# Performance work log

Hardware: AMD Instinct MI355X
Metric: run time of the kernel (lower is better)

Reference implementation:

```python
import jax, jax.numpy as jnp
import numpy as np
from jax.scipy.special import i0

# --- NUFFT adjoint (Kaiser-Bessel gridding) configuration ---
N = 512            # image side (image_shape)
K = 2 * N
M = 200_000        # n_measurements (visibilities)
B = 8              # batch of measurement vectors
J = 6              # gridding kernel width (plan uses (6, 6))
BETA = 2.34 * J


def setup_inputs() -> dict:
    key = jax.random.key(0)
    k1, k2, k3 = jax.random.split(key, 3)
    # uv coordinates in [-pi, pi) radians per pixel (standard NUFFT convention)
    uv = jax.random.uniform(k1, (M, 2), jnp.float32, -np.pi, np.pi)
    y_real = jax.random.normal(k2, (B, M), jnp.float32)
    y_imag = jax.random.normal(k3, (B, M), jnp.float32)
    weights = jnp.ones((M,), jnp.float32)  # measurement_weights
    return {"y_real": y_real, "y_imag": y_imag, "uv": uv, "weights": weights}


def _grid_1d(coord):
    """Per-axis gridding indices and Kaiser-Bessel weights.

    coord: (M,) frequencies in [-pi, pi). Returns idx (M, J) int32 grid
    columns (wrapped mod K) and w (M, J) float32 kernel weights.
    """
    k = coord / (2.0 * np.pi) * K            # grid units, in [-K/2, K/2)
    km = jnp.floor(k - J / 2.0)              # leftmost neighbor base
    j = jnp.arange(1, J + 1, dtype=k.dtype)
    pts = km[:, None] + j                    # (M, J) grid points covered
    d = k[:, None] - pts                     # signed distance, |d| <= J/2
    arg = jnp.maximum(1.0 - (2.0 * d / J) ** 2, 0.0)
    w = i0(BETA * jnp.sqrt(arg)) / i0(jnp.float32(BETA))
    idx = jnp.mod(pts, K).astype(jnp.int32)
    return idx, w.astype(jnp.float32)


def _deapod(n):
    """Gridding-correction (inverse FT of the KB kernel) at image pixels."""
    x = (jnp.arange(n, dtype=jnp.float32) - n / 2.0) / K
    t = BETA ** 2 - (np.pi * J * x) ** 2
    st = jnp.sqrt(jnp.abs(t))
    num = jnp.where(t > 0, jnp.sinh(st), jnp.sin(st))
    return num / jnp.maximum(st, 1e-6)


def reference(y_real, y_imag, uv, weights):
    y = (y_real + 1j * y_imag).astype(jnp.complex64) * weights  # (B, M)

    ix, wx = _grid_1d(uv[:, 0])  # (M, J)
    iy, wy = _grid_1d(uv[:, 1])  # (M, J)

    # Separable 6x6 kernel: outer products per measurement
    flat_idx = (ix[:, :, None] * K + iy[:, None, :]).reshape(-1)        # (M*J*J,)
    w2 = (wx[:, :, None] * wy[:, None, :]).reshape(M, J * J)            # (M, 36)
    vals = (y[:, :, None] * w2[None]).reshape(B, -1)                    # (B, M*36)

    # Scatter-add onto the oversampled grid (duplicate indices accumulate)
    grid = jnp.zeros((B, K * K), jnp.complex64).at[:, flat_idx].add(vals)
    grid = grid.reshape(B, K, K)

    # Unnormalized inverse FFT (adjoint of the forward FFT), shift to center
    img = jnp.fft.fftshift(jnp.fft.ifft2(grid), axes=(-2, -1)) * (K * K)

    # Crop central N x N region and de-apodize
    s = (K - N) // 2
    img_c = jnp.real(img[:, s:s + N, s:s + N])
    apod = _deapod(N)
    return img_c / (apod[:, None] * apod[None, :])
```

## Files before the change

### kernel.cpp

```cpp
#include <hip/hip_runtime.h>
#include <hip/hip_fp16.h>
#include <math.h>

#define KGRID 1024
#define NIMG  512
#define JW    6
#define BETAF 14.04f
#define NB    8
#define NBIN  16384
#define CAP   96

__device__ __forceinline__ float i0f_dev(float x) {
    float ax = fabsf(x);
    if (ax < 3.75f) {
        float z = ax * (1.0f / 3.75f);
        z = z * z;
        return 1.0f + z * (3.5156229f + z * (3.0899424f + z * (1.2067492f +
               z * (0.2659732f + z * (0.0360768f + z * 0.0045813f)))));
    } else {
        float z = 3.75f / ax;
        float p = 0.39894228f + z * (0.01328592f + z * (0.00225319f + z * (-0.00157565f +
                  z * (0.00916281f + z * (-0.02057706f + z * (0.02635537f +
                  z * (-0.01647633f + z * 0.00392377f)))))));
        return expf(ax) * rsqrtf(ax) * p;
    }
}

__global__ __launch_bounds__(256) void prep_kernel(
    const float* __restrict__ yr, const float* __restrict__ yi,
    const float* __restrict__ uv, const float* __restrict__ wts,
    float4* __restrict__ yF4, float4* __restrict__ pnt,
    int* __restrict__ cnt, int* __restrict__ list, int M)
{
    int m = blockIdx.x * 256 + threadIdx.x;
    if (m >= M) return;

    if (m == 0) {
        float4 z = make_float4(0.f, 0.f, 0.f, 0.f);
        #pragma unroll
        for (int q = 0; q < 4; q++) { pnt[(size_t)M * 4 + q] = z; yF4[(size_t)M * 4 + q] = z; }
    }

    float u = uv[2 * m], v = uv[2 * m + 1];
    const float c2g = (float)KGRID / 6.283185307179586f;
    float kx = u * c2g, ky = v * c2g;
    float kmx = floorf(kx - 3.0f), kmy = floorf(ky - 3.0f);
    int x0m = (((int)kmx + 1) + 1024) & 1023;
    int y0m = (((int)kmy + 1) + 1024) & 1023;

    int txA = x0m >> 3, txB = (txA + 1) & 127;
    int tyA = y0m >> 3, tyB = (tyA + 1) & 127;
    bool bx = (x0m & 7) >= 3;
    bool by = (y0m & 7) >= 3;
    int b0 = (txA << 7) | tyA;
    int b1 = (txA << 7) | tyB;
    int b2 = (txB << 7) | tyA;
    int b3 = (txB << 7) | tyB;
    int s0 = atomicAdd(&cnt[b0], 1);
    int s1 = by ? atomicAdd(&cnt[b1], 1) : -1;
    int s2 = bx ? atomicAdd(&cnt[b2], 1) : -1;
    int s3 = (bx && by) ? atomicAdd(&cnt[b3], 1) : -1;

    float inv = 1.0f / i0f_dev(BETAF);
    float s2c = inv * inv;
    float sc = wts[m] * s2c;

    float wx[JW], wy[JW];
    #pragma unroll
    for (int j = 0; j < JW; j++) {
        float dx = kx - kmx - 1.0f - (float)j;
        float rx = dx * (1.0f / 3.0f);
        float ax = fmaxf(1.0f - rx * rx, 0.0f);
        wx[j] = i0f_dev(BETAF * sqrtf(ax)) * sc;
        float dy = ky - kmy - 1.0f - (float)j;
        float ry = dy * (1.0f / 3.0f);
        float ay = fmaxf(1.0f - ry * ry, 0.0f);
        wy[j] = i0f_dev(BETAF * sqrtf(ay));
    }

    float4* p = pnt + (size_t)m * 4;
    p[0] = make_float4(wx[0], wx[1], wx[2], wx[3]);
    p[1] = make_float4(wx[4], wx[5], __int_as_float(x0m), __int_as_float(y0m));
    p[2] = make_float4(wy[0], wy[1], wy[2], wy[3]);
    p[3] = make_float4(wy[4], wy[5], 0.0f, 0.0f);

    #pragma unroll
    for (int bp = 0; bp < 4; bp++) {
        int bb = 2 * bp;
        yF4[(size_t)m * 4 + bp] = make_float4(
            yr[(size_t)bb * M + m],       yi[(size_t)bb * M + m],
            yr[(size_t)(bb + 1) * M + m], yi[(size_t)(bb + 1) * M + m]);
    }

    if ((unsigned)s0 < CAP) list[b0 * CAP + s0] = m;
    if ((unsigned)s1 < CAP) list[b1 * CAP + s1] = m;
    if ((unsigned)s2 < CAP) list[b2 * CAP + s2] = m;
    if ((unsigned)s3 < CAP) list[b3 * CAP + s3] = m;
}

__global__ __launch_bounds__(256) void grid_tile(
    const float* __restrict__ pnt1, const float4* __restrict__ yF4,
    const int* __restrict__ cnt, const int* __restrict__ list,
    __half2* __restrict__ gH, int M)
{
    int lane = threadIdx.x & 63;
    int wid  = threadIdx.x >> 6;
    int tile = blockIdx.x * 4 + wid;
    int tx0 = (tile >> 7) << 3;
    int ty0 = (tile & 127) << 3;
    int lx = lane >> 3, ly = lane & 7;
    int slot = lane & 15;

    float2 acc[NB];
    #pragma unroll
    for (int b = 0; b < NB; b++) acc[b] = make_float2(0.f, 0.f);

    int n = cnt[tile]; if (n > CAP) n = CAP;
    const int* lst = list + tile * CAP;

    int lv0 = (lane < n) ? lst[lane] : M;
    int lv1 = (64 + lane < n && 64 + lane < CAP) ? lst[64 + lane] : M;

    #define FETCH_M(i) __builtin_amdgcn_readlane(((i) < 64) ? lv0 : lv1, (i) & 63)

    int   mA = FETCH_M(0), mB = FETCH_M(1), mC = FETCH_M(2);
    float pwA = pnt1[(size_t)mA * 16 + slot];
    float pwB = pnt1[(size_t)mB * 16 + slot];
    float pwC = pnt1[(size_t)mC * 16 + slot];
    float4 yA0 = yF4[(size_t)mA * 4 + 0], yA1 = yF4[(size_t)mA * 4 + 1],
           yA2 = yF4[(size_t)mA * 4 + 2], yA3 = yF4[(size_t)mA * 4 + 3];
    float4 yB0 = yF4[(size_t)mB * 4 + 0], yB1 = yF4[(size_t)mB * 4 + 1],
           yB2 = yF4[(size_t)mB * 4 + 2], yB3 = yF4[(size_t)mB * 4 + 3];
    float4 yC0 = yF4[(size_t)mC * 4 + 0], yC1 = yF4[(size_t)mC * 4 + 1],
           yC2 = yF4[(size_t)mC * 4 + 2], yC3 = yF4[(size_t)mC * 4 + 3];

    for (int i = 0; i < n; i++) {
        int mD = FETCH_M(i + 3);
        float pwD = pnt1[(size_t)mD * 16 + slot];
        float4 yD0 = yF4[(size_t)mD * 4 + 0], yD1 = yF4[(size_t)mD * 4 + 1],
               yD2 = yF4[(size_t)mD * 4 + 2], yD3 = yF4[(size_t)mD * 4 + 3];

        int pwb = __float_as_int(pwA);
        int x0 = __builtin_amdgcn_readlane(pwb, 6);
        int y0 = __builtin_amdgcn_readlane(pwb, 7);
        int j1 = (tx0 + lx - x0) & 1023;
        int j2 = (ty0 + ly - y0) & 1023;
        int i1 = (j1 < 6) ? j1 : 15;
        int i2 = (j2 < 6) ? (j2 + 8) : 14;
        float wx = __int_as_float(__builtin_amdgcn_ds_bpermute(i1 << 2, pwb));
        float wy = __int_as_float(__builtin_amdgcn_ds_bpermute(i2 << 2, pwb));
        float w = wx * wy;

        acc[0].x = fmaf(w, yA0.x, acc[0].x); acc[0].y = fmaf(w, yA0.y, acc[0].y);
        acc[1].x = fmaf(w, yA0.z, acc[1].x); acc[1].y = fmaf(w, yA0.w, acc[1].y);
        acc[2].x = fmaf(w, yA1.x, acc[2].x); acc[2].y = fmaf(w, yA1.y, acc[2].y);
        acc[3].x = fmaf(w, yA1.z, acc[3].x); acc[3].y = fmaf(w, yA1.w, acc[3].y);
        acc[4].x = fmaf(w, yA2.x, acc[4].x); acc[4].y = fmaf(w, yA2.y, acc[4].y);
        acc[5].x = fmaf(w, yA2.z, acc[5].x); acc[5].y = fmaf(w, yA2.w, acc[5].y);
        acc[6].x = fmaf(w, yA3.x, acc[6].x); acc[6].y = fmaf(w, yA3.y, acc[6].y);
        acc[7].x = fmaf(w, yA3.z, acc[7].x); acc[7].y = fmaf(w, yA3.w, acc[7].y);

        pwA = pwB; yA0 = yB0; yA1 = yB1; yA2 = yB2; yA3 = yB3;
        pwB = pwC; yB0 = yC0; yB1 = yC1; yB2 = yC2; yB3 = yC3;
        pwC = pwD; yC0 = yD0; yC1 = yD1; yC2 = yD2; yC3 = yD3;
    }
    #undef FETCH_M

    size_t cell = ((size_t)(tx0 + lx) << 10) + (size_t)(ty0 + ly);
    #pragma unroll
    for (int b = 0; b < NB; b++)
        gH[((size_t)b << 20) + cell] = __float22half2_rn(acc[b]);
}

__device__ __forceinline__ void fft1024_inv(float2* X, float2* Y, const float2* W, int tid)
{
    float2* src = X;
    float2* dst = Y;
    #pragma unroll
    for (int stage = 0; stage < 10; stage++) {
        const int s = 1 << stage;
        __syncthreads();
        #pragma unroll
        for (int h = 0; h < 2; h++) {
            int t  = tid + (h << 8);
            int sp = t & ~(s - 1);
            float2 c0 = src[t];
            float2 c1 = src[t + 512];
            float2 sum = make_float2(c0.x + c1.x, c0.y + c1.y);
            float2 dif = make_float2(c0.x - c1.x, c0.y - c1.y);
            float2 w = W[sp];
            dst[t + sp]     = sum;
            dst[t + sp + s] = make_float2(w.x * dif.x - w.y * dif.y,
                                          w.x * dif.y + w.y * dif.x);
        }
        float2* tmp = src; src = dst; dst = tmp;
    }
    __syncthreads();
}

__global__ __launch_bounds__(256) void fft_pass1(const __half2* __restrict__ gH,
                                                 __half2* __restrict__ T)
{
    __shared__ float2 A[1024];
    __shared__ float2 Bb[1024];
    __shared__ float2 W[512];
    __shared__ __half2 R[8][512];

    int blk = blockIdx.x;
    int p   = blk >> 7;
    int g   = blk & 127;
    int tid = threadIdx.x;

    #pragma unroll
    for (int h = 0; h < 2; h++) {
        int j = tid + (h << 8);
        float sn, cn;
        __sincosf(6.283185307179586f * (float)j * (1.0f / 1024.0f), &sn, &cn);
        W[j] = make_float2(cn, sn);
    }

    const __half2* gA = gH + ((size_t)(2 * p)     << 20);
    const __half2* gB = gH + ((size_t)(2 * p + 1) << 20);

    for (int f = 0; f < 8; f++) {
        int k1  = (f < 4) ? (4 * g + f) : (1020 - 4 * g + (f - 4));
        int nk1 = (1024 - k1) & 1023;
        const __half2* rA  = gA + ((size_t)k1  << 10);
        const __half2* rAn = gA + ((size_t)nk1 << 10);
        const __half2* rB  = gB + ((size_t)k1  << 10);
        const __half2* rBn = gB + ((size_t)nk1 << 10);
        __syncthreads();
        #pragma unroll
        for (int h = 0; h < 4; h++) {
            int k2  = tid + (h << 8);
            int nk2 = (1024 - k2) & 1023;
            float2 va  = __half22float2(rA[k2]);
            float2 van = __half22float2(rAn[nk2]);
            float2 vb  = __half22float2(rB[k2]);
            float2 vbn = __half22float2(rBn[nk2]);
            A[k2] = make_float2(0.5f * (va.x + van.x) - 0.5f * (vb.y - vbn.y),
                                0.5f * (va.y - van.y) + 0.5f * (vb.x + vbn.x));
        }
        fft1024_inv(A, Bb, W, tid);
        #pragma unroll
        for (int h = 0; h < 2; h++) {
            int xo2 = tid + (h << 8);
            R[f][xo2] = __float22half2_rn(A[(xo2 + 768) & 1023]);
        }
    }
    __syncthreads();

    #pragma unroll
    for (int h = 0; h < 2; h++) {
        int xo2 = tid + (h << 8);
        __half2* Trow = T + (((size_t)p * 512 + xo2) << 10);
        int4 q0, q1;
        q0.x = *(const int*)&R[0][xo2]; q0.y = *(const int*)&R[1][xo2];
        q0.z = *(const int*)&R[2][xo2]; q0.w = *(const int*)&R[3][xo2];
        q1.x = *(const int*)&R[4][xo2]; q1.y = *(const int*)&R[5][xo2];
        q1.z = *(const int*)&R[6][xo2]; q1.w = *(const int*)&R[7][xo2];
        *(int4*)(Trow + 4 * g)          = q0;
        *(int4*)(Trow + (1020 - 4 * g)) = q1;
    }
}

__device__ __forceinline__ float apodf(int n) {
    float x  = ((float)n - 256.0f) * (1.0f / 1024.0f);
    float px = 3.14159265358979f * 6.0f * x;
    float t  = BETAF * BETAF - px * px;
    float st = sqrtf(fabsf(t));
    float num = (t > 0.0f) ? sinhf(st) : __sinf(st);
    return num / fmaxf(st, 1e-6f);
}

__global__ __launch_bounds__(256) void fft_pass2(const __half2* __restrict__ T,
                                                 float* __restrict__ out)
{
    __shared__ float2 A[1024];
    __shared__ float2 Bb[1024];
    __shared__ float2 W[512];
    __shared__ float2 R[4][512];

    int blk = blockIdx.x;
    int p   = blk >> 7;
    int xg  = blk & 127;
    int tid = threadIdx.x;

    #pragma unroll
    for (int h = 0; h < 2; h++) {
        int j = tid + (h << 8);
        float sn, cn;
        __sincosf(6.283185307179586f * (float)j * (1.0f / 1024.0f), &sn, &cn);
        W[j] = make_float2(cn, sn);
    }

    float a2[4];
    #pragma unroll
    for (int r = 0; r < 4; r++) a2[r] = apodf((xg << 2) + r);

    for (int r = 0; r < 4; r++) {
        int xo2 = (xg << 2) + r;
        const __half2* row = T + (((size_t)p * 512 + xo2) << 10);
        __syncthreads();
        #pragma unroll
        for (int h = 0; h < 4; h++) {
            int i = tid + (h << 8);
            A[i] = __half22float2(row[i]);
        }
        fft1024_inv(A, Bb, W, tid);
        #pragma unroll
        for (int h = 0; h < 2; h++) {
            int xo1 = tid + (h << 8);
            float2 v = A[(xo1 + 768) & 1023];
            R[r][xo1] = make_float2(v.x / a2[r], v.y / a2[r]);
        }
    }
    __syncthreads();

    int b0 = 2 * p;
    #pragma unroll
    for (int h = 0; h < 2; h++) {
        int xo1 = tid + (h << 8);
        float inva1 = 1.0f / apodf(xo1);
        float2 f0 = R[0][xo1], f1 = R[1][xo1], f2 = R[2][xo1], f3 = R[3][xo1];
        float4* o0 = (float4*)(out + (((size_t)b0 * 512 + xo1) << 9) + (xg << 2));
        float4* o1 = (float4*)(out + (((size_t)(b0 + 1) * 512 + xo1) << 9) + (xg << 2));
        *o0 = make_float4(f0.x * inva1, f1.x * inva1, f2.x * inva1, f3.x * inva1);
        *o1 = make_float4(f0.y * inva1, f1.y * inva1, f2.y * inva1, f3.y * inva1);
    }
}

extern "C" void kernel_launch(void* const* d_in, const int* in_sizes, int n_in,
                              void* d_out, int out_size, void* d_ws, size_t ws_size,
                              hipStream_t stream)
{
    const float* yr  = (const float*)d_in[0];
    const float* yi  = (const float*)d_in[1];
    const float* uv  = (const float*)d_in[2];
    const float* wts = (const float*)d_in[3];

    int M = in_sizes[3];

    __half2* gH = (__half2*)d_ws;
    __half2* T  = (__half2*)((char*)d_ws + ((size_t)32 << 20));
    char*    p2 = (char*)d_ws + ((size_t)64 << 20);
    int*    cnt  = (int*)p2;
    int*    list = (int*)(p2 + 65536);
    float4* yF4  = (float4*)(p2 + 6553600);
    float4* pnt  = (float4*)(p2 + 19500032);

    hipMemsetAsync(cnt, 0, NBIN * sizeof(int), stream);
    prep_kernel<<<dim3((M + 255) / 256), dim3(256), 0, stream>>>(
        yr, yi, uv, wts, yF4, pnt, cnt, list, M);
    grid_tile<<<dim3(NBIN / 4), dim3(256), 0, stream>>>(
        (const float*)pnt, (const float4*)yF4, cnt, list, gH, M);
    fft_pass1<<<dim3(4 * 128), dim3(256), 0, stream>>>(gH, T);
    fft_pass2<<<dim3(4 * 128), dim3(256), 0, stream>>>(T, (float*)d_out);
}
```

Baseline: 188.9 us.

## Store gridding inputs in half precision and use radix-4 FFT with two rows per block

Per-point kernel weights and weighted measurements are now packed as fp16 in prep_kernel, which halves the gather traffic in grid_tile. The weights are folded into y, and the grid offsets are stored as half floats. The FFT moves from ten radix-2 stages to five radix-4 stages, and each 512-thread block transforms two rows at once. This cuts the number of syncthreads and shared-memory passes. The cost is lower accuracy: the weights, the y values and the grid offsets (integers up to 1023, which fp16 holds exactly) are all in half precision.

```diff
diff --git a/kernel.cpp b/kernel.cpp
--- a/kernel.cpp
+++ b/kernel.cpp
@@ -29,16 +29,16 @@
 __global__ __launch_bounds__(256) void prep_kernel(
     const float* __restrict__ yr, const float* __restrict__ yi,
     const float* __restrict__ uv, const float* __restrict__ wts,
-    float4* __restrict__ yF4, float4* __restrict__ pnt,
+    int4* __restrict__ yH, int4* __restrict__ pntH,
     int* __restrict__ cnt, int* __restrict__ list, int M)
 {
     int m = blockIdx.x * 256 + threadIdx.x;
     if (m >= M) return;
 
     if (m == 0) {
-        float4 z = make_float4(0.f, 0.f, 0.f, 0.f);
-        #pragma unroll
-        for (int q = 0; q < 4; q++) { pnt[(size_t)M * 4 + q] = z; yF4[(size_t)M * 4 + q] = z; }
+        int4 z = make_int4(0, 0, 0, 0);
+        yH[2 * (size_t)M] = z; yH[2 * (size_t)M + 1] = z;
+        pntH[2 * (size_t)M] = z; pntH[2 * (size_t)M + 1] = z;
     }
 
     float u = uv[2 * m], v = uv[2 * m + 1];
@@ -62,35 +62,34 @@
     int s3 = (bx && by) ? atomicAdd(&cnt[b3], 1) : -1;
 
     float inv = 1.0f / i0f_dev(BETAF);
-    float s2c = inv * inv;
-    float sc = wts[m] * s2c;
-
-    float wx[JW], wy[JW];
+
+    __half hx[16] __attribute__((aligned(16)));
     #pragma unroll
     for (int j = 0; j < JW; j++) {
         float dx = kx - kmx - 1.0f - (float)j;
         float rx = dx * (1.0f / 3.0f);
         float ax = fmaxf(1.0f - rx * rx, 0.0f);
-        wx[j] = i0f_dev(BETAF * sqrtf(ax)) * sc;
+        hx[j] = __float2half_rn(i0f_dev(BETAF * sqrtf(ax)) * inv);
         float dy = ky - kmy - 1.0f - (float)j;
         float ry = dy * (1.0f / 3.0f);
         float ay = fmaxf(1.0f - ry * ry, 0.0f);
-        wy[j] = i0f_dev(BETAF * sqrtf(ay));
-    }
-
-    float4* p = pnt + (size_t)m * 4;
-    p[0] = make_float4(wx[0], wx[1], wx[2], wx[3]);
-    p[1] = make_float4(wx[4], wx[5], __int_as_float(x0m), __int_as_float(y0m));
-    p[2] = make_float4(wy[0], wy[1], wy[2], wy[3]);
-    p[3] = make_float4(wy[4], wy[5], 0.0f, 0.0f);
-
-    #pragma unroll
-    for (int bp = 0; bp < 4; bp++) {
-        int bb = 2 * bp;
-        yF4[(size_t)m * 4 + bp] = make_float4(
-            yr[(size_t)bb * M + m],       yi[(size_t)bb * M + m],
-            yr[(size_t)(bb + 1) * M + m], yi[(size_t)(bb + 1) * M + m]);
-    }
+        hx[8 + j] = __float2half_rn(i0f_dev(BETAF * sqrtf(ay)) * inv);
+    }
+    hx[6] = __float2half_rn((float)x0m);
+    hx[7] = __float2half_rn((float)y0m);
+    hx[14] = __float2half_rn(0.0f);
+    hx[15] = __float2half_rn(0.0f);
+    pntH[2 * (size_t)m]     = *(const int4*)&hx[0];
+    pntH[2 * (size_t)m + 1] = *(const int4*)&hx[8];
+
+    float wm = wts[m];
+    __half2 yh[8] __attribute__((aligned(16)));
+    #pragma unroll
+    for (int b = 0; b < NB; b++)
+        yh[b] = __float22half2_rn(make_float2(yr[(size_t)b * M + m] * wm,
+                                              yi[(size_t)b * M + m] * wm));
+    yH[2 * (size_t)m]     = *(const int4*)&yh[0];
+    yH[2 * (size_t)m + 1] = *(const int4*)&yh[4];
 
     if ((unsigned)s0 < CAP) list[b0 * CAP + s0] = m;
     if ((unsigned)s1 < CAP) list[b1 * CAP + s1] = m;
@@ -99,7 +98,7 @@
 }
 
 __global__ __launch_bounds__(256) void grid_tile(
-    const float* __restrict__ pnt1, const float4* __restrict__ yF4,
+    const __half* __restrict__ pnt1, const int4* __restrict__ yH,
     const int* __restrict__ cnt, const int* __restrict__ list,
     __half2* __restrict__ gH, int M)
 {
@@ -122,27 +121,25 @@
     int lv1 = (64 + lane < n && 64 + lane < CAP) ? lst[64 + lane] : M;
 
     #define FETCH_M(i) __builtin_amdgcn_readlane(((i) < 64) ? lv0 : lv1, (i) & 63)
-
-    int   mA = FETCH_M(0), mB = FETCH_M(1), mC = FETCH_M(2);
-    float pwA = pnt1[(size_t)mA * 16 + slot];
-    float pwB = pnt1[(size_t)mB * 16 + slot];
-    float pwC = pnt1[(size_t)mC * 16 + slot];
-    float4 yA0 = yF4[(size_t)mA * 4 + 0], yA1 = yF4[(size_t)mA * 4 + 1],
-           yA2 = yF4[(size_t)mA * 4 + 2], yA3 = yF4[(size_t)mA * 4 + 3];
-    float4 yB0 = yF4[(size_t)mB * 4 + 0], yB1 = yF4[(size_t)mB * 4 + 1],
-           yB2 = yF4[(size_t)mB * 4 + 2], yB3 = yF4[(size_t)mB * 4 + 3];
-    float4 yC0 = yF4[(size_t)mC * 4 + 0], yC1 = yF4[(size_t)mC * 4 + 1],
-           yC2 = yF4[(size_t)mC * 4 + 2], yC3 = yF4[(size_t)mC * 4 + 3];
+    #define ACC(k, word) { __half2 hh = *(__half2*)&(word); float2 ff = __half22float2(hh); \
+                           acc[k].x = fmaf(w, ff.x, acc[k].x); acc[k].y = fmaf(w, ff.y, acc[k].y); }
+
+    int mA = FETCH_M(0), mB = FETCH_M(1), mC = FETCH_M(2);
+    float pwA = __half2float(pnt1[(size_t)mA * 16 + slot]);
+    float pwB = __half2float(pnt1[(size_t)mB * 16 + slot]);
+    float pwC = __half2float(pnt1[(size_t)mC * 16 + slot]);
+    int4 uA0 = yH[2 * (size_t)mA], uA1 = yH[2 * (size_t)mA + 1];
+    int4 uB0 = yH[2 * (size_t)mB], uB1 = yH[2 * (size_t)mB + 1];
+    int4 uC0 = yH[2 * (size_t)mC], uC1 = yH[2 * (size_t)mC + 1];
 
     for (int i = 0; i < n; i++) {
         int mD = FETCH_M(i + 3);
-        float pwD = pnt1[(size_t)mD * 16 + slot];
-        float4 yD0 = yF4[(size_t)mD * 4 + 0], yD1 = yF4[(size_t)mD * 4 + 1],
-               yD2 = yF4[(size_t)mD * 4 + 2], yD3 = yF4[(size_t)mD * 4 + 3];
+        float pwD = __half2float(pnt1[(size_t)mD * 16 + slot]);
+        int4 uD0 = yH[2 * (size_t)mD], uD1 = yH[2 * (size_t)mD + 1];
 
         int pwb = __float_as_int(pwA);
-        int x0 = __builtin_amdgcn_readlane(pwb, 6);
-        int y0 = __builtin_amdgcn_readlane(pwb, 7);
+        int x0 = (int)__int_as_float(__builtin_amdgcn_readlane(pwb, 6));
+        int y0 = (int)__int_as_float(__builtin_amdgcn_readlane(pwb, 7));
         int j1 = (tx0 + lx - x0) & 1023;
         int j2 = (ty0 + ly - y0) & 1023;
         int i1 = (j1 < 6) ? j1 : 15;
@@ -151,19 +148,14 @@
         float wy = __int_as_float(__builtin_amdgcn_ds_bpermute(i2 << 2, pwb));
         float w = wx * wy;
 
-        acc[0].x = fmaf(w, yA0.x, acc[0].x); acc[0].y = fmaf(w, yA0.y, acc[0].y);
-        acc[1].x = fmaf(w, yA0.z, acc[1].x); acc[1].y = fmaf(w, yA0.w, acc[1].y);
-        acc[2].x = fmaf(w, yA1.x, acc[2].x); acc[2].y = fmaf(w, yA1.y, acc[2].y);
-        acc[3].x = fmaf(w, yA1.z, acc[3].x); acc[3].y = fmaf(w, yA1.w, acc[3].y);
-        acc[4].x = fmaf(w, yA2.x, acc[4].x); acc[4].y = fmaf(w, yA2.y, acc[4].y);
-        acc[5].x = fmaf(w, yA2.z, acc[5].x); acc[5].y = fmaf(w, yA2.w, acc[5].y);
-        acc[6].x = fmaf(w, yA3.x, acc[6].x); acc[6].y = fmaf(w, yA3.y, acc[6].y);
-        acc[7].x = fmaf(w, yA3.z, acc[7].x); acc[7].y = fmaf(w, yA3.w, acc[7].y);
-
-        pwA = pwB; yA0 = yB0; yA1 = yB1; yA2 = yB2; yA3 = yB3;
-        pwB = pwC; yB0 = yC0; yB1 = yC1; yB2 = yC2; yB3 = yC3;
-        pwC = pwD; yC0 = yD0; yC1 = yD1; yC2 = yD2; yC3 = yD3;
-    }
+        ACC(0, uA0.x) ACC(1, uA0.y) ACC(2, uA0.z) ACC(3, uA0.w)
+        ACC(4, uA1.x) ACC(5, uA1.y) ACC(6, uA1.z) ACC(7, uA1.w)
+
+        pwA = pwB; uA0 = uB0; uA1 = uB1;
+        pwB = pwC; uB0 = uC0; uB1 = uC1;
+        pwC = pwD; uC0 = uD0; uC1 = uD1;
+    }
+    #undef ACC
     #undef FETCH_M
 
     size_t cell = ((size_t)(tx0 + lx) << 10) + (size_t)(ty0 + ly);
@@ -172,37 +164,52 @@
         gH[((size_t)b << 20) + cell] = __float22half2_rn(acc[b]);
 }
 
-__device__ __forceinline__ void fft1024_inv(float2* X, float2* Y, const float2* W, int tid)
+__device__ __forceinline__ float2 cmulf(float2 a, float2 b) {
+    return make_float2(a.x * b.x - a.y * b.y, a.x * b.y + a.y * b.x);
+}
+
+__device__ __forceinline__ float2* fft1024_r4(float2* X, float2* Y, const float2* W, int lt)
 {
     float2* src = X;
     float2* dst = Y;
     #pragma unroll
-    for (int stage = 0; stage < 10; stage++) {
-        const int s = 1 << stage;
+    for (int st = 0; st < 5; st++) {
+        const int s = 1 << (2 * st);
         __syncthreads();
-        #pragma unroll
-        for (int h = 0; h < 2; h++) {
-            int t  = tid + (h << 8);
-            int sp = t & ~(s - 1);
-            float2 c0 = src[t];
-            float2 c1 = src[t + 512];
-            float2 sum = make_float2(c0.x + c1.x, c0.y + c1.y);
-            float2 dif = make_float2(c0.x - c1.x, c0.y - c1.y);
-            float2 w = W[sp];
-            dst[t + sp]     = sum;
-            dst[t + sp + s] = make_float2(w.x * dif.x - w.y * dif.y,
-                                          w.x * dif.y + w.y * dif.x);
-        }
-        float2* tmp = src; src = dst; dst = tmp;
+        int r  = lt & (s - 1);
+        int qs = lt - r;
+        float2 a0 = src[lt];
+        float2 a1 = src[lt + 256];
+        float2 a2 = src[lt + 512];
+        float2 a3 = src[lt + 768];
+        float2 e02 = make_float2(a0.x + a2.x, a0.y + a2.y);
+        float2 d02 = make_float2(a0.x - a2.x, a0.y - a2.y);
+        float2 e13 = make_float2(a1.x + a3.x, a1.y + a3.y);
+        float2 d13 = make_float2(a1.x - a3.x, a1.y - a3.y);
+        float2 y0 = make_float2(e02.x + e13.x, e02.y + e13.y);
+        float2 y2 = make_float2(e02.x - e13.x, e02.y - e13.y);
+        float2 id = make_float2(-d13.y, d13.x);
+        float2 y1 = make_float2(d02.x + id.x, d02.y + id.y);
+        float2 y3 = make_float2(d02.x - id.x, d02.y - id.y);
+        float2 w1 = W[qs];
+        float2 w2 = W[2 * qs];
+        float2 w3 = cmulf(w1, w2);
+        int base = 4 * qs + r;
+        dst[base]         = y0;
+        dst[base + s]     = cmulf(y1, w1);
+        dst[base + 2 * s] = cmulf(y2, w2);
+        dst[base + 3 * s] = cmulf(y3, w3);
+        float2* t = src; src = dst; dst = t;
     }
     __syncthreads();
-}
-
-__global__ __launch_bounds__(256) void fft_pass1(const __half2* __restrict__ gH,
+    return src;
+}
+
+__global__ __launch_bounds__(512) void fft_pass1(const __half2* __restrict__ gH,
                                                  __half2* __restrict__ T)
 {
-    __shared__ float2 A[1024];
-    __shared__ float2 Bb[1024];
+    __shared__ float2 A[2][1024];
+    __shared__ float2 Bb[2][1024];
     __shared__ float2 W[512];
     __shared__ __half2 R[8][512];
 
@@ -210,20 +217,21 @@
     int p   = blk >> 7;
     int g   = blk & 127;
     int tid = threadIdx.x;
-
-    #pragma unroll
-    for (int h = 0; h < 2; h++) {
-        int j = tid + (h << 8);
+    int sub = tid >> 8;
+    int lt  = tid & 255;
+
+    {
         float sn, cn;
-        __sincosf(6.283185307179586f * (float)j * (1.0f / 1024.0f), &sn, &cn);
-        W[j] = make_float2(cn, sn);
+        __sincosf(6.283185307179586f * (float)tid * (1.0f / 1024.0f), &sn, &cn);
+        W[tid] = make_float2(cn, sn);
     }
 
     const __half2* gA = gH + ((size_t)(2 * p)     << 20);
     const __half2* gB = gH + ((size_t)(2 * p + 1) << 20);
 
-    for (int f = 0; f < 8; f++) {
-        int k1  = (f < 4) ? (4 * g + f) : (1020 - 4 * g + (f - 4));
+    for (int rr = 0; rr < 4; rr++) {
+        int f  = rr + 4 * sub;
+        int k1 = (sub == 0) ? (4 * g + rr) : (1020 - 4 * g + rr);
         int nk1 = (1024 - k1) & 1023;
         const __half2* rA  = gA + ((size_t)k1  << 10);
         const __half2* rAn = gA + ((size_t)nk1 << 10);
@@ -232,27 +240,26 @@
         __syncthreads();
         #pragma unroll
         for (int h = 0; h < 4; h++) {
-            int k2  = tid + (h << 8);
+            int k2  = lt + (h << 8);
             int nk2 = (1024 - k2) & 1023;
             float2 va  = __half22float2(rA[k2]);
             float2 van = __half22float2(rAn[nk2]);
             float2 vb  = __half22float2(rB[k2]);
             float2 vbn = __half22float2(rBn[nk2]);
-            A[k2] = make_float2(0.5f * (va.x + van.x) - 0.5f * (vb.y - vbn.y),
-                                0.5f * (va.y - van.y) + 0.5f * (vb.x + vbn.x));
+            A[sub][k2] = make_float2(0.5f * (va.x + van.x) - 0.5f * (vb.y - vbn.y),
+                                     0.5f * (va.y - van.y) + 0.5f * (vb.x + vbn.x));
         }
-        fft1024_inv(A, Bb, W, tid);
+        float2* res = fft1024_r4(A[sub], Bb[sub], W, lt);
         #pragma unroll
         for (int h = 0; h < 2; h++) {
-            int xo2 = tid + (h << 8);
-            R[f][xo2] = __float22half2_rn(A[(xo2 + 768) & 1023]);
+            int xo2 = lt + (h << 8);
+            R[f][xo2] = __float22half2_rn(res[(xo2 + 768) & 1023]);
         }
     }
     __syncthreads();
 
-    #pragma unroll
-    for (int h = 0; h < 2; h++) {
-        int xo2 = tid + (h << 8);
+    {
+        int xo2 = tid;
         __half2* Trow = T + (((size_t)p * 512 + xo2) << 10);
         int4 q0, q1;
         q0.x = *(const int*)&R[0][xo2]; q0.y = *(const int*)&R[1][xo2];
@@ -273,11 +280,11 @@
     return num / fmaxf(st, 1e-6f);
 }
 
-__global__ __launch_bounds__(256) void fft_pass2(const __half2* __restrict__ T,
+__global__ __launch_bounds__(512) void fft_pass2(const __half2* __restrict__ T,
                                                  float* __restrict__ out)
 {
-    __shared__ float2 A[1024];
-    __shared__ float2 Bb[1024];
+    __shared__ float2 A[2][1024];
+    __shared__ float2 Bb[2][1024];
     __shared__ float2 W[512];
     __shared__ float2 R[4][512];
 
@@ -285,42 +292,39 @@
     int p   = blk >> 7;
     int xg  = blk & 127;
     int tid = threadIdx.x;
-
-    #pragma unroll
-    for (int h = 0; h < 2; h++) {
-        int j = tid + (h << 8);
+    int sub = tid >> 8;
+    int lt  = tid & 255;
+
+    {
         float sn, cn;
-        __sincosf(6.283185307179586f * (float)j * (1.0f / 1024.0f), &sn, &cn);
-        W[j] = make_float2(cn, sn);
-    }
-
-    float a2[4];
-    #pragma unroll
-    for (int r = 0; r < 4; r++) a2[r] = apodf((xg << 2) + r);
-
-    for (int r = 0; r < 4; r++) {
-        int xo2 = (xg << 2) + r;
+        __sincosf(6.283185307179586f * (float)tid * (1.0f / 1024.0f), &sn, &cn);
+        W[tid] = make_float2(cn, sn);
+    }
+
+    for (int rr = 0; rr < 2; rr++) {
+        int c   = 2 * rr + sub;
+        int xo2 = (xg << 2) + c;
         const __half2* row = T + (((size_t)p * 512 + xo2) << 10);
         __syncthreads();
         #pragma unroll
         for (int h = 0; h < 4; h++) {
-            int i = tid + (h << 8);
-            A[i] = __half22float2(row[i]);
+            int i = lt + (h << 8);
+            A[sub][i] = __half22float2(row[i]);
         }
-        fft1024_inv(A, Bb, W, tid);
+        float2* res = fft1024_r4(A[sub], Bb[sub], W, lt);
+        float a2v = apodf(xo2);
         #pragma unroll
         for (int h = 0; h < 2; h++) {
-            int xo1 = tid + (h << 8);
-            float2 v = A[(xo1 + 768) & 1023];
-            R[r][xo1] = make_float2(v.x / a2[r], v.y / a2[r]);
+            int xo1 = lt + (h << 8);
+            float2 v = res[(xo1 + 768) & 1023];
+            R[c][xo1] = make_float2(v.x / a2v, v.y / a2v);
         }
     }
     __syncthreads();
 
     int b0 = 2 * p;
-    #pragma unroll
-    for (int h = 0; h < 2; h++) {
-        int xo1 = tid + (h << 8);
+    {
+        int xo1 = tid;
         float inva1 = 1.0f / apodf(xo1);
         float2 f0 = R[0][xo1], f1 = R[1][xo1], f2 = R[2][xo1], f3 = R[3][xo1];
         float4* o0 = (float4*)(out + (((size_t)b0 * 512 + xo1) << 9) + (xg << 2));
@@ -344,16 +348,16 @@
     __half2* gH = (__half2*)d_ws;
     __half2* T  = (__half2*)((char*)d_ws + ((size_t)32 << 20));
     char*    p2 = (char*)d_ws + ((size_t)64 << 20);
-    int*    cnt  = (int*)p2;
-    int*    list = (int*)(p2 + 65536);
-    float4* yF4  = (float4*)(p2 + 6553600);
-    float4* pnt  = (float4*)(p2 + 19500032);
+    int*   cnt  = (int*)p2;
+    int*   list = (int*)(p2 + 65536);
+    int4*  yH   = (int4*)(p2 + ((size_t)8 << 20));
+    int4*  pntH = (int4*)(p2 + ((size_t)16 << 20));
 
     hipMemsetAsync(cnt, 0, NBIN * sizeof(int), stream);
     prep_kernel<<<dim3((M + 255) / 256), dim3(256), 0, stream>>>(
-        yr, yi, uv, wts, yF4, pnt, cnt, list, M);
+        yr, yi, uv, wts, yH, pntH, cnt, list, M);
     grid_tile<<<dim3(NBIN / 4), dim3(256), 0, stream>>>(
-        (const float*)pnt, (const float4*)yF4, cnt, list, gH, M);
-    fft_pass1<<<dim3(4 * 128), dim3(256), 0, stream>>>(gH, T);
-    fft_pass2<<<dim3(4 * 128), dim3(256), 0, stream>>>(T, (float*)d_out);
-}
+        (const __half*)pntH, (const int4*)yH, cnt, list, gH, M);
+    fft_pass1<<<dim3(4 * 128), dim3(512), 0, stream>>>(gH, T);
+    fft_pass2<<<dim3(4 * 128), dim3(512), 0, stream>>>(T, (float*)d_out);
+}
```

After: 189.3 us. About the same (+0.2%).
